# Kernel optimization log

Measured on AMD Instinct MI355X. Metric: run time of the kernel, lower is better.

Reference implementation:

```python
import jax, jax.numpy as jnp
import numpy as np

N_EMBD = 1024
NUM_EXPERTS = 8
TOP_K = 2
HIDDEN = 2048  # n_embd * hidden_mult(2)
AUX_COEF = 0.01
B, S = 4, 2048


def setup_inputs() -> dict:
    key = jax.random.key(0)
    k_x, k_g, k_w1, k_w2 = jax.random.split(key, 4)
    x = jax.random.normal(k_x, (B, S, N_EMBD), dtype=jnp.float32)
    # router gate: Linear(n_embd, num_experts, bias=False) -> weight (E, D), applied as x @ W^T
    gate_w = jax.random.uniform(k_g, (NUM_EXPERTS, N_EMBD), dtype=jnp.float32,
                                minval=-1.0 / np.sqrt(N_EMBD), maxval=1.0 / np.sqrt(N_EMBD))
    w1 = jax.random.uniform(k_w1, (NUM_EXPERTS, N_EMBD, HIDDEN), dtype=jnp.float32,
                            minval=-1.0 / np.sqrt(N_EMBD), maxval=1.0 / np.sqrt(N_EMBD))
    w2 = jax.random.uniform(k_w2, (NUM_EXPERTS, HIDDEN, N_EMBD), dtype=jnp.float32,
                            minval=-1.0 / np.sqrt(HIDDEN), maxval=1.0 / np.sqrt(HIDDEN))
    return {"x": x, "gate_w": gate_w, "w1": w1, "w2": w2}


def reference(x, gate_w, w1, w2):
    batch, seq, d = x.shape
    # router (token-level, no noise / eval path)
    router_logits = jnp.einsum('bsd,ed->bse', x, gate_w)          # (B,S,E)
    router_probs = jax.nn.softmax(router_logits, axis=-1)
    top_k_probs, top_k_indices = jax.lax.top_k(router_probs, TOP_K)  # (B,S,K)
    top_k_probs = top_k_probs / jnp.sum(top_k_probs, axis=-1, keepdims=True)

    # dense all-expert FFN (matches torch einsum pattern)
    x_flat = x.reshape(-1, d)                                      # (N,D), N=B*S
    hidden = jnp.einsum('nd,edh->neh', x_flat, w1)                 # (N,E,H)
    hidden = jax.nn.relu(hidden)
    expert_out = jnp.einsum('neh,ehd->ned', hidden, w2)            # (N,E,D)
    expert_out = expert_out.reshape(batch, seq, NUM_EXPERTS, d)    # (B,S,E,D)

    # gather selected experts and combine
    idx = top_k_indices[..., None]                                 # (B,S,K,1)
    selected = jnp.take_along_axis(expert_out, idx, axis=2)        # (B,S,K,D)
    output = jnp.sum(selected * top_k_probs[..., None], axis=2)    # (B,S,D)

    # load-balancing aux loss (Switch style)
    probs_flat = router_probs.reshape(-1, NUM_EXPERTS)             # (N,E)
    top_expert = jnp.argmax(probs_flat, axis=-1)                   # (N,)
    f = jnp.mean(jax.nn.one_hot(top_expert, NUM_EXPERTS, dtype=probs_flat.dtype), axis=0)
    P = jnp.mean(probs_flat, axis=0)
    aux_loss = AUX_COEF * NUM_EXPERTS * jnp.sum(f * P)
    return output, aux_loss
```

## Files before the change

kernel.cpp:

```cpp
#include <hip/hip_runtime.h>
#include <hip/hip_bf16.h>
#include <stdint.h>

#define N_TOK 8192
#define DIM   1024
#define HID   2048
#define NEXP  8
#define RB    256

typedef __bf16 bf16x8 __attribute__((ext_vector_type(8)));
typedef float  f32x4  __attribute__((ext_vector_type(4)));
typedef unsigned short u16x8 __attribute__((ext_vector_type(8)));
typedef unsigned short u16x4 __attribute__((ext_vector_type(4)));

__device__ __forceinline__ float bits2f(unsigned short u) {
    union { unsigned int i; float f; } c; c.i = ((unsigned int)u) << 16; return c.f;
}
__device__ __forceinline__ unsigned short f2bfbits(float f) {
    __hip_bfloat16 h = __float2bfloat16(f);
    return *(unsigned short*)&h;
}

__device__ __forceinline__ void load_lds16(const void* g, void* l) {
    __builtin_amdgcn_global_load_lds(
        (const __attribute__((address_space(1))) void*)g,
        (__attribute__((address_space(3))) void*)l,
        16, 0, 0);
}

__global__ __launch_bounds__(512) void route_k(
    const float* __restrict__ x,
    const float* __restrict__ gate,
    int* __restrict__ epack, float* __restrict__ pw,
    unsigned short* __restrict__ xb,
    int* __restrict__ H0, int* __restrict__ H1, float* __restrict__ Pblk)
{
    __shared__ float gwS[NEXP][16][64];
    __shared__ int h0S[NEXP], h1S[NEXP];
    __shared__ float pS[NEXP];
    int tid = threadIdx.x;
    if (tid < NEXP) { h0S[tid] = 0; h1S[tid] = 0; pS[tid] = 0.f; }
    for (int idx = tid; idx < NEXP * DIM; idx += 512) {
        int e = idx >> 10, rem = idx & 1023, i = rem >> 6, l = rem & 63;
        gwS[e][i][l] = gate[e * DIM + l * 16 + i];
    }
    __syncthreads();
    int w = tid >> 6, lane = tid & 63;
    float prAcc[NEXP];
    #pragma unroll
    for (int e = 0; e < NEXP; ++e) prAcc[e] = 0.f;
    for (int it = 0; it < 4; ++it) {
        int token = blockIdx.x * 32 + w * 4 + it;
        const float* xr = x + (size_t)token * DIM + lane * 16;
        float xv[16];
        #pragma unroll
        for (int q = 0; q < 4; ++q) {
            float4 v = *(const float4*)(xr + q * 4);
            xv[q * 4 + 0] = v.x; xv[q * 4 + 1] = v.y; xv[q * 4 + 2] = v.z; xv[q * 4 + 3] = v.w;
        }
        {
            u16x8 o0, o1;
            #pragma unroll
            for (int i = 0; i < 8; ++i) { o0[i] = f2bfbits(xv[i]); o1[i] = f2bfbits(xv[8 + i]); }
            unsigned short* dst = xb + (size_t)token * DIM + lane * 16;
            *(u16x8*)dst = o0;
            *(u16x8*)(dst + 8) = o1;
        }
        float lg[NEXP];
        #pragma unroll
        for (int e = 0; e < NEXP; ++e) {
            float s = 0.f;
            #pragma unroll
            for (int i = 0; i < 16; ++i) s += xv[i] * gwS[e][i][lane];
            lg[e] = s;
        }
        #pragma unroll
        for (int off = 32; off > 0; off >>= 1)
            #pragma unroll
            for (int e = 0; e < NEXP; ++e) lg[e] += __shfl_xor(lg[e], off);
        float mx = lg[0]; int am = 0;
        #pragma unroll
        for (int e = 1; e < NEXP; ++e) if (lg[e] > mx) { mx = lg[e]; am = e; }
        float pr[NEXP], se = 0.f;
        #pragma unroll
        for (int e = 0; e < NEXP; ++e) { pr[e] = __expf(lg[e] - mx); se += pr[e]; }
        float inv = 1.f / se;
        #pragma unroll
        for (int e = 0; e < NEXP; ++e) pr[e] *= inv;
        float m2 = -1.f; int a2 = 0;
        #pragma unroll
        for (int e = 0; e < NEXP; ++e) if (e != am && pr[e] > m2) { m2 = pr[e]; a2 = e; }
        float psum = pr[am] + m2;
        if (lane == 0) {
            epack[token] = am | (a2 << 4);
            pw[token * 2] = pr[am] / psum;
            pw[token * 2 + 1] = m2 / psum;
            atomicAdd(&h0S[am], 1);
            atomicAdd(&h1S[a2], 1);
            #pragma unroll
            for (int e = 0; e < NEXP; ++e) prAcc[e] += pr[e];
        }
    }
    if (lane == 0) {
        #pragma unroll
        for (int e = 0; e < NEXP; ++e) atomicAdd(&pS[e], prAcc[e]);
    }
    __syncthreads();
    if (tid < NEXP) {
        H0[blockIdx.x * NEXP + tid] = h0S[tid];
        H1[blockIdx.x * NEXP + tid] = h1S[tid];
        Pblk[blockIdx.x * NEXP + tid] = pS[tid];
    }
}

__global__ __launch_bounds__(256) void scan_k(
    const int* __restrict__ H0, const int* __restrict__ H1,
    const float* __restrict__ Pblk,
    int* __restrict__ bbL, int* __restrict__ counts, int* __restrict__ basep,
    float* __restrict__ aux)
{
    __shared__ int h0S[RB * NEXP], h1S[RB * NEXP], bbS[RB * NEXP];
    __shared__ float pSh[RB * NEXP];
    __shared__ int cS[NEXP], fS[NEXP];
    __shared__ float psS[NEXP];
    int tid = threadIdx.x;
    for (int i = tid; i < RB * NEXP; i += 256) { h0S[i] = H0[i]; h1S[i] = H1[i]; pSh[i] = Pblk[i]; }
    __syncthreads();
    if (tid < NEXP) {
        int run = 0, f = 0; float p = 0.f;
        for (int b = 0; b < RB; ++b) {
            int i = b * NEXP + tid;
            bbS[i] = run;
            run += h0S[i] + h1S[i];
            f += h0S[i];
            p += pSh[i];
        }
        cS[tid] = run; fS[tid] = f; psS[tid] = p;
        counts[tid] = run;
    }
    __syncthreads();
    if (tid == 0) {
        int b = 0; float s = 0.f;
        for (int e = 0; e < NEXP; ++e) {
            basep[e] = b; b += cS[e];
            s += (fS[e] * (1.f / 8192.f)) * (psS[e] * (1.f / 8192.f));
        }
        aux[0] = 0.01f * 8.f * s;
    }
    __syncthreads();
    for (int i = tid; i < RB * NEXP; i += 256) bbL[i] = bbS[i];
}

__global__ __launch_bounds__(256) void scatter_k(
    const int* __restrict__ epack, const int* __restrict__ bbL,
    int* __restrict__ tok_list, int* __restrict__ code)
{
    int tid = threadIdx.x;
    int w = tid >> 6, lane = tid & 63;
    int g = blockIdx.x * 4 + w;
    int token = g * 32 + (lane >> 1);
    int ep = epack[token];
    int e = (lane & 1) ? ((ep >> 4) & 0xF) : (ep & 0xF);
    unsigned long long lower = (lane == 0) ? 0ull : ((~0ull) >> (64 - lane));
    unsigned long long mymask = 0;
    #pragma unroll
    for (int ee = 0; ee < NEXP; ++ee) {
        unsigned long long m = __ballot(e == ee);
        if (ee == e) mymask = m;
    }
    int rank = __popcll(mymask & lower);
    int slot = bbL[g * NEXP + e] + rank;
    tok_list[e * N_TOK + slot] = token;
    code[token * 2 + (lane & 1)] = (e << 13) | slot;
}

__global__ __launch_bounds__(256) void transpose_cvt_k(const float* __restrict__ in,
                                                       unsigned short* __restrict__ out,
                                                       int R, int C)
{
    __shared__ unsigned short tile[64][72];
    int e = blockIdx.z;
    const float* inp = in + (size_t)e * R * C;
    unsigned short* outp = out + (size_t)e * R * C;
    int r0 = blockIdx.y * 64, c0 = blockIdx.x * 64;
    int tid = threadIdx.x;
    {
        int r = tid >> 2;
        int cseg = (tid & 3) * 16;
        const float* src = inp + (size_t)(r0 + r) * C + c0 + cseg;
        #pragma unroll
        for (int q = 0; q < 4; ++q) {
            float4 v = *(const float4*)(src + q * 4);
            tile[r][cseg + q * 4 + 0] = f2bfbits(v.x);
            tile[r][cseg + q * 4 + 1] = f2bfbits(v.y);
            tile[r][cseg + q * 4 + 2] = f2bfbits(v.z);
            tile[r][cseg + q * 4 + 3] = f2bfbits(v.w);
        }
    }
    __syncthreads();
    {
        int c = tid >> 2;
        int rseg = (tid & 3) * 16;
        unsigned short* dst = outp + (size_t)(c0 + c) * R + r0 + rseg;
        #pragma unroll
        for (int h = 0; h < 2; ++h) {
            u16x8 o;
            #pragma unroll
            for (int i = 0; i < 8; ++i) o[i] = tile[rseg + h * 8 + i][c];
            *(u16x8*)(dst + h * 8) = o;
        }
    }
}

template<bool GATHER, bool RELU, bool SPLITK>
__global__ __launch_bounds__(256) void moe_gemm(
    const unsigned short* __restrict__ A,
    const unsigned short* __restrict__ B,
    unsigned short* __restrict__ O0,
    unsigned short* __restrict__ O1,
    const int* __restrict__ counts,
    const int* __restrict__ basep,
    const int* __restrict__ tok_list,
    const int K, const int N)
{
    int e, koff, steps;
    unsigned short* O;
    if (SPLITK) {
        e = blockIdx.z >> 1;
        int kp = blockIdx.z & 1;
        koff = kp * (K >> 1);
        steps = K >> 6;
        O = kp ? O1 : O0;
    } else {
        e = blockIdx.z; koff = 0; steps = K >> 5; O = O0;
    }
    const int cnt = counts[e];
    const int m0 = blockIdx.y * 128;
    if (m0 >= cnt) return;
    const int n0 = blockIdx.x * 128;
    const int bas = basep[e];

    const int tid = threadIdx.x;
    const int w = tid >> 6, lane = tid & 63;
    const int wr = w >> 1, wc = w & 1;

    __shared__ __align__(16) unsigned short lds[8192];

    const int kc = ((tid & 3) ^ ((tid >> 3) & 3)) * 8;
    const int r0i = tid >> 2, r1i = 64 + (tid >> 2);
    const unsigned short *aRow0, *aRow1;
    if (GATHER) {
        int s0 = m0 + r0i, s1 = m0 + r1i;
        int t0 = (s0 < cnt) ? tok_list[e * N_TOK + s0] : 0;
        int t1 = (s1 < cnt) ? tok_list[e * N_TOK + s1] : 0;
        aRow0 = A + (size_t)t0 * K + koff + kc;
        aRow1 = A + (size_t)t1 * K + koff + kc;
    } else {
        int s0 = m0 + r0i; if (s0 > cnt - 1) s0 = cnt - 1;
        int s1 = m0 + r1i; if (s1 > cnt - 1) s1 = cnt - 1;
        aRow0 = A + (size_t)(bas + s0) * K + koff + kc;
        aRow1 = A + (size_t)(bas + s1) * K + koff + kc;
    }
    const unsigned short* Be = B + (size_t)e * N * K;
    const unsigned short* bRow0 = Be + (size_t)(n0 + r0i) * K + koff + kc;
    const unsigned short* bRow1 = Be + (size_t)(n0 + r1i) * K + koff + kc;

    f32x4 acc[4][4];
    #pragma unroll
    for (int i = 0; i < 4; ++i)
        #pragma unroll
        for (int j = 0; j < 4; ++j) acc[i][j] = f32x4{0.f, 0.f, 0.f, 0.f};

    const int quad = lane >> 4, ml = lane & 15;
    unsigned short* ldsA0 = &lds[tid * 8];
    unsigned short* ldsA1 = &lds[2048 + tid * 8];
    unsigned short* ldsB0 = &lds[4096 + tid * 8];
    unsigned short* ldsB1 = &lds[6144 + tid * 8];

    int offA[4], offB[4];
    #pragma unroll
    for (int i = 0; i < 4; ++i) {
        int Ra = wr * 64 + i * 16 + ml;
        offA[i] = Ra * 32 + ((quad ^ ((Ra >> 1) & 3)) * 8);
        int Rb = wc * 64 + i * 16 + ml;
        offB[i] = 4096 + Rb * 32 + ((quad ^ ((Rb >> 1) & 3)) * 8);
    }

    for (int kt = 0; kt < steps; ++kt) {
        const int ko = kt * 32;
        load_lds16(aRow0 + ko, ldsA0);
        load_lds16(aRow1 + ko, ldsA1);
        load_lds16(bRow0 + ko, ldsB0);
        load_lds16(bRow1 + ko, ldsB1);
        __syncthreads();
        bf16x8 af[4], bfr[4];
        #pragma unroll
        for (int i = 0; i < 4; ++i) af[i] = *(const bf16x8*)&lds[offA[i]];
        #pragma unroll
        for (int j = 0; j < 4; ++j) bfr[j] = *(const bf16x8*)&lds[offB[j]];
        #pragma unroll
        for (int i = 0; i < 4; ++i)
            #pragma unroll
            for (int j = 0; j < 4; ++j)
                acc[i][j] = __builtin_amdgcn_mfma_f32_16x16x32_bf16(af[i], bfr[j], acc[i][j], 0, 0, 0);
        __syncthreads();
    }

    #pragma unroll
    for (int i = 0; i < 4; ++i) {
        int rbase = wr * 64 + i * 16 + quad * 4;
        #pragma unroll
        for (int r = 0; r < 4; ++r) {
            int slot = m0 + rbase + r;
            if (slot < cnt) {
                unsigned short* orow = O + (size_t)(bas + slot) * N + n0 + wc * 64 + ml;
                #pragma unroll
                for (int j = 0; j < 4; ++j) {
                    float v = acc[i][j][r];
                    if (RELU) v = v > 0.f ? v : 0.f;
                    orow[j * 16] = f2bfbits(v);
                }
            }
        }
    }
}

__global__ __launch_bounds__(256) void combine_k(
    const unsigned short* __restrict__ Y0,
    const unsigned short* __restrict__ Y1,
    const int* __restrict__ code, const float* __restrict__ pw,
    const int* __restrict__ basep,
    float* __restrict__ out)
{
    int t = blockIdx.x;
    int c0 = code[t * 2], c1 = code[t * 2 + 1];
    float p0 = pw[t * 2], p1 = pw[t * 2 + 1];
    size_t r0 = (size_t)(basep[c0 >> 13] + (c0 & 0x1FFF)) * DIM;
    size_t r1 = (size_t)(basep[c1 >> 13] + (c1 & 0x1FFF)) * DIM;
    int d = threadIdx.x * 4;
    u16x4 a0 = *(const u16x4*)(Y0 + r0 + d);
    u16x4 a1 = *(const u16x4*)(Y1 + r0 + d);
    u16x4 b0 = *(const u16x4*)(Y0 + r1 + d);
    u16x4 b1 = *(const u16x4*)(Y1 + r1 + d);
    float4 o;
    o.x = p0 * (bits2f(a0[0]) + bits2f(a1[0])) + p1 * (bits2f(b0[0]) + bits2f(b1[0]));
    o.y = p0 * (bits2f(a0[1]) + bits2f(a1[1])) + p1 * (bits2f(b0[1]) + bits2f(b1[1]));
    o.z = p0 * (bits2f(a0[2]) + bits2f(a1[2])) + p1 * (bits2f(b0[2]) + bits2f(b1[2]));
    o.w = p0 * (bits2f(a0[3]) + bits2f(a1[3])) + p1 * (bits2f(b0[3]) + bits2f(b1[3]));
    *(float4*)(out + (size_t)t * DIM + d) = o;
}

extern "C" void kernel_launch(void* const* d_in, const int* in_sizes, int n_in,
                              void* d_out, int out_size, void* d_ws, size_t ws_size,
                              hipStream_t stream)
{
    const float* x    = (const float*)d_in[0];
    const float* gate = (const float*)d_in[1];
    const float* w1   = (const float*)d_in[2];
    const float* w2   = (const float*)d_in[3];
    float* out = (float*)d_out;

    char* ws = (char*)d_ws;
    int*   counts   = (int*)(ws + 0);
    int*   basep    = (int*)(ws + 256);
    int*   epack    = (int*)(ws + 1024);
    int*   H0       = (int*)(ws + 1024 + 32768);
    int*   H1       = (int*)(ws + 1024 + 40960);
    float* Pblk     = (float*)(ws + 1024 + 49152);
    int*   bbL      = (int*)(ws + 1024 + 57344);
    int*   tok_list = (int*)(ws + 131072);
    int*   code     = (int*)(ws + 131072 + 262144);
    float* pw       = (float*)(ws + 131072 + 262144 + 65536);
    unsigned short* w1t    = (unsigned short*)(ws + (1 << 20));
    unsigned short* w2t    = (unsigned short*)(ws + (1 << 20) + 33554432);
    unsigned short* hidden = (unsigned short*)(ws + (1 << 20) + 67108864);
    unsigned short* xb     = (unsigned short*)(ws + (1 << 20) + 134217728);
    unsigned short* Yp0    = xb;
    unsigned short* Yp1    = w1t;

    route_k<<<RB, 512, 0, stream>>>(x, gate, epack, pw, xb, H0, H1, Pblk);
    scan_k<<<1, 256, 0, stream>>>(H0, H1, Pblk, bbL, counts, basep, out + (size_t)N_TOK * DIM);
    scatter_k<<<64, 256, 0, stream>>>(epack, bbL, tok_list, code);
    transpose_cvt_k<<<dim3(HID / 64, DIM / 64, NEXP), 256, 0, stream>>>(w1, w1t, DIM, HID);
    transpose_cvt_k<<<dim3(DIM / 64, HID / 64, NEXP), 256, 0, stream>>>(w2, w2t, HID, DIM);
    moe_gemm<true, true, false><<<dim3(HID / 128, 64, NEXP), 256, 0, stream>>>(
        xb, w1t, hidden, nullptr, counts, basep, tok_list, DIM, HID);
    moe_gemm<false, false, true><<<dim3(DIM / 128, 64, NEXP * 2), 256, 0, stream>>>(
        hidden, w2t, Yp0, Yp1, counts, basep, tok_list, HID, DIM);
    combine_k<<<N_TOK, 256, 0, stream>>>(Yp0, Yp1, code, pw, basep, out);
}
```

Baseline: 428.8 us.

## Fuse routing with weight transposes and pipeline GEMM loads with double-buffered LDS

Routing and both weight transpose/bf16 conversions are merged into one kernel launch so they share a grid and drop two launches. The MoE GEMM gets a double-buffered 64-wide K pipeline using async global-to-LDS loads with explicit vmcnt waits, raw barriers and MFMA priority boosting. Split-K on the second GEMM is removed, so combine reads one partial instead of two. The larger LDS (64KB) limits occupancy, and dropping split-K halves the grid for the down projection.

Result: faster. 399.0 us (-7.0%).

```diff
diff --git a/kernel.cpp b/kernel.cpp
--- a/kernel.cpp
+++ b/kernel.cpp
@@ -28,88 +28,137 @@
         16, 0, 0);
 }
 
-__global__ __launch_bounds__(512) void route_k(
+__global__ __launch_bounds__(256) void fused_pre_k(
     const float* __restrict__ x,
     const float* __restrict__ gate,
+    const float* __restrict__ w1,
+    const float* __restrict__ w2,
     int* __restrict__ epack, float* __restrict__ pw,
     unsigned short* __restrict__ xb,
-    int* __restrict__ H0, int* __restrict__ H1, float* __restrict__ Pblk)
-{
-    __shared__ float gwS[NEXP][16][64];
-    __shared__ int h0S[NEXP], h1S[NEXP];
-    __shared__ float pS[NEXP];
-    int tid = threadIdx.x;
-    if (tid < NEXP) { h0S[tid] = 0; h1S[tid] = 0; pS[tid] = 0.f; }
-    for (int idx = tid; idx < NEXP * DIM; idx += 512) {
-        int e = idx >> 10, rem = idx & 1023, i = rem >> 6, l = rem & 63;
-        gwS[e][i][l] = gate[e * DIM + l * 16 + i];
+    int* __restrict__ H0, int* __restrict__ H1, float* __restrict__ Pblk,
+    unsigned short* __restrict__ w1t, unsigned short* __restrict__ w2t)
+{
+    __shared__ __align__(16) union {
+        struct { float gw[NEXP][16][64]; int h0[NEXP]; int h1[NEXP]; float p[NEXP]; } r;
+        unsigned short tile[64][72];
+    } S;
+    const int tid = threadIdx.x;
+    const int bx  = blockIdx.x;
+
+    if (bx < RB) {
+        if (tid < NEXP) { S.r.h0[tid] = 0; S.r.h1[tid] = 0; S.r.p[tid] = 0.f; }
+        for (int idx = tid; idx < NEXP * DIM; idx += 256) {
+            int e = idx >> 10, rem = idx & 1023, i = rem >> 6, l = rem & 63;
+            S.r.gw[e][i][l] = gate[e * DIM + l * 16 + i];
+        }
+        __syncthreads();
+        int w = tid >> 6, lane = tid & 63;
+        float prAcc[NEXP];
+        #pragma unroll
+        for (int e = 0; e < NEXP; ++e) prAcc[e] = 0.f;
+        for (int it = 0; it < 8; ++it) {
+            int token = bx * 32 + w * 8 + it;
+            const float* xr = x + (size_t)token * DIM + lane * 16;
+            float xv[16];
+            #pragma unroll
+            for (int q = 0; q < 4; ++q) {
+                float4 v = *(const float4*)(xr + q * 4);
+                xv[q * 4 + 0] = v.x; xv[q * 4 + 1] = v.y; xv[q * 4 + 2] = v.z; xv[q * 4 + 3] = v.w;
+            }
+            {
+                u16x8 o0, o1;
+                #pragma unroll
+                for (int i = 0; i < 8; ++i) { o0[i] = f2bfbits(xv[i]); o1[i] = f2bfbits(xv[8 + i]); }
+                unsigned short* dst = xb + (size_t)token * DIM + lane * 16;
+                *(u16x8*)dst = o0;
+                *(u16x8*)(dst + 8) = o1;
+            }
+            float lg[NEXP];
+            #pragma unroll
+            for (int e = 0; e < NEXP; ++e) {
+                float s = 0.f;
+                #pragma unroll
+                for (int i = 0; i < 16; ++i) s += xv[i] * S.r.gw[e][i][lane];
+                lg[e] = s;
+            }
+            #pragma unroll
+            for (int off = 32; off > 0; off >>= 1)
+                #pragma unroll
+                for (int e = 0; e < NEXP; ++e) lg[e] += __shfl_xor(lg[e], off);
+            float mx = lg[0]; int am = 0;
+            #pragma unroll
+            for (int e = 1; e < NEXP; ++e) if (lg[e] > mx) { mx = lg[e]; am = e; }
+            float pr[NEXP], se = 0.f;
+            #pragma unroll
+            for (int e = 0; e < NEXP; ++e) { pr[e] = __expf(lg[e] - mx); se += pr[e]; }
+            float inv = 1.f / se;
+            #pragma unroll
+            for (int e = 0; e < NEXP; ++e) pr[e] *= inv;
+            float m2 = -1.f; int a2 = 0;
+            #pragma unroll
+            for (int e = 0; e < NEXP; ++e) if (e != am && pr[e] > m2) { m2 = pr[e]; a2 = e; }
+            float psum = pr[am] + m2;
+            if (lane == 0) {
+                epack[token] = am | (a2 << 4);
+                pw[token * 2] = pr[am] / psum;
+                pw[token * 2 + 1] = m2 / psum;
+                atomicAdd(&S.r.h0[am], 1);
+                atomicAdd(&S.r.h1[a2], 1);
+                #pragma unroll
+                for (int e = 0; e < NEXP; ++e) prAcc[e] += pr[e];
+            }
+        }
+        if (lane == 0) {
+            #pragma unroll
+            for (int e = 0; e < NEXP; ++e) atomicAdd(&S.r.p[e], prAcc[e]);
+        }
+        __syncthreads();
+        if (tid < NEXP) {
+            H0[bx * NEXP + tid] = S.r.h0[tid];
+            H1[bx * NEXP + tid] = S.r.h1[tid];
+            Pblk[bx * NEXP + tid] = S.r.p[tid];
+        }
+        return;
+    }
+
+    int bT = bx - RB;
+    const float* inp; unsigned short* outp;
+    int R, C, r0, c0;
+    if (bT < 4096) {
+        int e = bT >> 9, rem = bT & 511;
+        R = DIM; C = HID;
+        inp = w1 + (size_t)e * R * C; outp = w1t + (size_t)e * R * C;
+        r0 = (rem >> 5) << 6; c0 = (rem & 31) << 6;
+    } else {
+        int b2 = bT - 4096;
+        int e = b2 >> 9, rem = b2 & 511;
+        R = HID; C = DIM;
+        inp = w2 + (size_t)e * R * C; outp = w2t + (size_t)e * R * C;
+        r0 = (rem >> 4) << 6; c0 = (rem & 15) << 6;
+    }
+    {
+        int r = tid >> 2, cseg = (tid & 3) * 16;
+        const float* src = inp + (size_t)(r0 + r) * C + c0 + cseg;
+        #pragma unroll
+        for (int q = 0; q < 4; ++q) {
+            float4 v = *(const float4*)(src + q * 4);
+            S.tile[r][cseg + q * 4 + 0] = f2bfbits(v.x);
+            S.tile[r][cseg + q * 4 + 1] = f2bfbits(v.y);
+            S.tile[r][cseg + q * 4 + 2] = f2bfbits(v.z);
+            S.tile[r][cseg + q * 4 + 3] = f2bfbits(v.w);
+        }
     }
     __syncthreads();
-    int w = tid >> 6, lane = tid & 63;
-    float prAcc[NEXP];
-    #pragma unroll
-    for (int e = 0; e < NEXP; ++e) prAcc[e] = 0.f;
-    for (int it = 0; it < 4; ++it) {
-        int token = blockIdx.x * 32 + w * 4 + it;
-        const float* xr = x + (size_t)token * DIM + lane * 16;
-        float xv[16];
-        #pragma unroll
-        for (int q = 0; q < 4; ++q) {
-            float4 v = *(const float4*)(xr + q * 4);
-            xv[q * 4 + 0] = v.x; xv[q * 4 + 1] = v.y; xv[q * 4 + 2] = v.z; xv[q * 4 + 3] = v.w;
-        }
-        {
-            u16x8 o0, o1;
-            #pragma unroll
-            for (int i = 0; i < 8; ++i) { o0[i] = f2bfbits(xv[i]); o1[i] = f2bfbits(xv[8 + i]); }
-            unsigned short* dst = xb + (size_t)token * DIM + lane * 16;
-            *(u16x8*)dst = o0;
-            *(u16x8*)(dst + 8) = o1;
-        }
-        float lg[NEXP];
-        #pragma unroll
-        for (int e = 0; e < NEXP; ++e) {
-            float s = 0.f;
-            #pragma unroll
-            for (int i = 0; i < 16; ++i) s += xv[i] * gwS[e][i][lane];
-            lg[e] = s;
-        }
-        #pragma unroll
-        for (int off = 32; off > 0; off >>= 1)
-            #pragma unroll
-            for (int e = 0; e < NEXP; ++e) lg[e] += __shfl_xor(lg[e], off);
-        float mx = lg[0]; int am = 0;
-        #pragma unroll
-        for (int e = 1; e < NEXP; ++e) if (lg[e] > mx) { mx = lg[e]; am = e; }
-        float pr[NEXP], se = 0.f;
-        #pragma unroll
-        for (int e = 0; e < NEXP; ++e) { pr[e] = __expf(lg[e] - mx); se += pr[e]; }
-        float inv = 1.f / se;
-        #pragma unroll
-        for (int e = 0; e < NEXP; ++e) pr[e] *= inv;
-        float m2 = -1.f; int a2 = 0;
-        #pragma unroll
-        for (int e = 0; e < NEXP; ++e) if (e != am && pr[e] > m2) { m2 = pr[e]; a2 = e; }
-        float psum = pr[am] + m2;
-        if (lane == 0) {
-            epack[token] = am | (a2 << 4);
-            pw[token * 2] = pr[am] / psum;
-            pw[token * 2 + 1] = m2 / psum;
-            atomicAdd(&h0S[am], 1);
-            atomicAdd(&h1S[a2], 1);
-            #pragma unroll
-            for (int e = 0; e < NEXP; ++e) prAcc[e] += pr[e];
-        }
-    }
-    if (lane == 0) {
-        #pragma unroll
-        for (int e = 0; e < NEXP; ++e) atomicAdd(&pS[e], prAcc[e]);
-    }
-    __syncthreads();
-    if (tid < NEXP) {
-        H0[blockIdx.x * NEXP + tid] = h0S[tid];
-        H1[blockIdx.x * NEXP + tid] = h1S[tid];
-        Pblk[blockIdx.x * NEXP + tid] = pS[tid];
+    {
+        int c = tid >> 2, rseg = (tid & 3) * 16;
+        unsigned short* dst = outp + (size_t)(c0 + c) * R + r0 + rseg;
+        #pragma unroll
+        for (int h = 0; h < 2; ++h) {
+            u16x8 o;
+            #pragma unroll
+            for (int i = 0; i < 8; ++i) o[i] = S.tile[rseg + h * 8 + i][c];
+            *(u16x8*)(dst + h * 8) = o;
+        }
     }
 }
 
@@ -174,66 +223,21 @@
     code[token * 2 + (lane & 1)] = (e << 13) | slot;
 }
 
-__global__ __launch_bounds__(256) void transpose_cvt_k(const float* __restrict__ in,
-                                                       unsigned short* __restrict__ out,
-                                                       int R, int C)
-{
-    __shared__ unsigned short tile[64][72];
-    int e = blockIdx.z;
-    const float* inp = in + (size_t)e * R * C;
-    unsigned short* outp = out + (size_t)e * R * C;
-    int r0 = blockIdx.y * 64, c0 = blockIdx.x * 64;
-    int tid = threadIdx.x;
-    {
-        int r = tid >> 2;
-        int cseg = (tid & 3) * 16;
-        const float* src = inp + (size_t)(r0 + r) * C + c0 + cseg;
-        #pragma unroll
-        for (int q = 0; q < 4; ++q) {
-            float4 v = *(const float4*)(src + q * 4);
-            tile[r][cseg + q * 4 + 0] = f2bfbits(v.x);
-            tile[r][cseg + q * 4 + 1] = f2bfbits(v.y);
-            tile[r][cseg + q * 4 + 2] = f2bfbits(v.z);
-            tile[r][cseg + q * 4 + 3] = f2bfbits(v.w);
-        }
-    }
-    __syncthreads();
-    {
-        int c = tid >> 2;
-        int rseg = (tid & 3) * 16;
-        unsigned short* dst = outp + (size_t)(c0 + c) * R + r0 + rseg;
-        #pragma unroll
-        for (int h = 0; h < 2; ++h) {
-            u16x8 o;
-            #pragma unroll
-            for (int i = 0; i < 8; ++i) o[i] = tile[rseg + h * 8 + i][c];
-            *(u16x8*)(dst + h * 8) = o;
-        }
-    }
-}
-
-template<bool GATHER, bool RELU, bool SPLITK>
-__global__ __launch_bounds__(256) void moe_gemm(
+#define VMW(Nv) asm volatile("s_waitcnt vmcnt(" #Nv ")" ::: "memory")
+#define BARv()  asm volatile("s_barrier" ::: "memory")
+
+template<bool GATHER, bool RELU, int KT>
+__global__ __launch_bounds__(256, 2) void moe_gemm(
     const unsigned short* __restrict__ A,
     const unsigned short* __restrict__ B,
-    unsigned short* __restrict__ O0,
-    unsigned short* __restrict__ O1,
+    unsigned short* __restrict__ O,
     const int* __restrict__ counts,
     const int* __restrict__ basep,
     const int* __restrict__ tok_list,
-    const int K, const int N)
-{
-    int e, koff, steps;
-    unsigned short* O;
-    if (SPLITK) {
-        e = blockIdx.z >> 1;
-        int kp = blockIdx.z & 1;
-        koff = kp * (K >> 1);
-        steps = K >> 6;
-        O = kp ? O1 : O0;
-    } else {
-        e = blockIdx.z; koff = 0; steps = K >> 5; O = O0;
-    }
+    const int N)
+{
+    constexpr int K = KT * 64;
+    const int e = blockIdx.z;
     const int cnt = counts[e];
     const int m0 = blockIdx.y * 128;
     if (m0 >= cnt) return;
@@ -244,7 +248,7 @@
     const int w = tid >> 6, lane = tid & 63;
     const int wr = w >> 1, wc = w & 1;
 
-    __shared__ __align__(16) unsigned short lds[8192];
+    __shared__ __align__(16) unsigned short lds[32768];
 
     const int kc = ((tid & 3) ^ ((tid >> 3) & 3)) * 8;
     const int r0i = tid >> 2, r1i = 64 + (tid >> 2);
@@ -253,17 +257,17 @@
         int s0 = m0 + r0i, s1 = m0 + r1i;
         int t0 = (s0 < cnt) ? tok_list[e * N_TOK + s0] : 0;
         int t1 = (s1 < cnt) ? tok_list[e * N_TOK + s1] : 0;
-        aRow0 = A + (size_t)t0 * K + koff + kc;
-        aRow1 = A + (size_t)t1 * K + koff + kc;
+        aRow0 = A + (size_t)t0 * K + kc;
+        aRow1 = A + (size_t)t1 * K + kc;
     } else {
         int s0 = m0 + r0i; if (s0 > cnt - 1) s0 = cnt - 1;
         int s1 = m0 + r1i; if (s1 > cnt - 1) s1 = cnt - 1;
-        aRow0 = A + (size_t)(bas + s0) * K + koff + kc;
-        aRow1 = A + (size_t)(bas + s1) * K + koff + kc;
+        aRow0 = A + (size_t)(bas + s0) * K + kc;
+        aRow1 = A + (size_t)(bas + s1) * K + kc;
     }
     const unsigned short* Be = B + (size_t)e * N * K;
-    const unsigned short* bRow0 = Be + (size_t)(n0 + r0i) * K + koff + kc;
-    const unsigned short* bRow1 = Be + (size_t)(n0 + r1i) * K + koff + kc;
+    const unsigned short* bRow0 = Be + (size_t)(n0 + r0i) * K + kc;
+    const unsigned short* bRow1 = Be + (size_t)(n0 + r1i) * K + kc;
 
     f32x4 acc[4][4];
     #pragma unroll
@@ -272,38 +276,56 @@
         for (int j = 0; j < 4; ++j) acc[i][j] = f32x4{0.f, 0.f, 0.f, 0.f};
 
     const int quad = lane >> 4, ml = lane & 15;
-    unsigned short* ldsA0 = &lds[tid * 8];
-    unsigned short* ldsA1 = &lds[2048 + tid * 8];
-    unsigned short* ldsB0 = &lds[4096 + tid * 8];
-    unsigned short* ldsB1 = &lds[6144 + tid * 8];
-
     int offA[4], offB[4];
     #pragma unroll
     for (int i = 0; i < 4; ++i) {
         int Ra = wr * 64 + i * 16 + ml;
         offA[i] = Ra * 32 + ((quad ^ ((Ra >> 1) & 3)) * 8);
         int Rb = wc * 64 + i * 16 + ml;
-        offB[i] = 4096 + Rb * 32 + ((quad ^ ((Rb >> 1) & 3)) * 8);
-    }
-
-    for (int kt = 0; kt < steps; ++kt) {
-        const int ko = kt * 32;
-        load_lds16(aRow0 + ko, ldsA0);
-        load_lds16(aRow1 + ko, ldsA1);
-        load_lds16(bRow0 + ko, ldsB0);
-        load_lds16(bRow1 + ko, ldsB1);
-        __syncthreads();
+        offB[i] = Rb * 32 + ((quad ^ ((Rb >> 1) & 3)) * 8);
+    }
+
+    auto stageG = [&](int tt, int h) {
+        const int db = ((tt & 1) << 14) + (h << 12) + (tid << 3);
+        const int toff = tt * 64 + h * 32;
+        load_lds16(aRow0 + toff, &lds[db]);
+        load_lds16(aRow1 + toff, &lds[db + 2048]);
+        load_lds16(bRow0 + toff, &lds[db + 8192]);
+        load_lds16(bRow1 + toff, &lds[db + 8192 + 2048]);
+    };
+
+    auto compute = [&](int bb, int ks) {
+        const unsigned short* Lb = &lds[(bb << 14) + (ks << 12)];
         bf16x8 af[4], bfr[4];
         #pragma unroll
-        for (int i = 0; i < 4; ++i) af[i] = *(const bf16x8*)&lds[offA[i]];
-        #pragma unroll
-        for (int j = 0; j < 4; ++j) bfr[j] = *(const bf16x8*)&lds[offB[j]];
+        for (int i = 0; i < 4; ++i) af[i] = *(const bf16x8*)&Lb[offA[i]];
+        #pragma unroll
+        for (int j = 0; j < 4; ++j) bfr[j] = *(const bf16x8*)&Lb[8192 + offB[j]];
+        __builtin_amdgcn_s_setprio(1);
         #pragma unroll
         for (int i = 0; i < 4; ++i)
             #pragma unroll
             for (int j = 0; j < 4; ++j)
                 acc[i][j] = __builtin_amdgcn_mfma_f32_16x16x32_bf16(af[i], bfr[j], acc[i][j], 0, 0, 0);
-        __syncthreads();
+        __builtin_amdgcn_s_setprio(0);
+        BARv();
+    };
+
+    stageG(0, 0); stageG(0, 1); stageG(1, 0);
+
+    #pragma unroll 2
+    for (int t = 0; t < KT - 2; ++t) {
+        const int b = t & 1;
+        stageG(t + 1, 1); VMW(12); BARv(); compute(b, 0);
+        stageG(t + 2, 0); VMW(12); BARv(); compute(b, 1);
+    }
+    {
+        const int bA = (KT - 2) & 1;
+        stageG(KT - 1, 1); VMW(12); BARv(); compute(bA, 0);
+        VMW(8);  BARv(); compute(bA, 1);
+        const int bB = (KT - 1) & 1;
+        VMW(4);  BARv(); compute(bB, 0);
+        VMW(0);  BARv(); compute(bB, 1);
     }
 
     #pragma unroll
@@ -326,8 +348,7 @@
 }
 
 __global__ __launch_bounds__(256) void combine_k(
-    const unsigned short* __restrict__ Y0,
-    const unsigned short* __restrict__ Y1,
+    const unsigned short* __restrict__ Y,
     const int* __restrict__ code, const float* __restrict__ pw,
     const int* __restrict__ basep,
     float* __restrict__ out)
@@ -338,15 +359,13 @@
     size_t r0 = (size_t)(basep[c0 >> 13] + (c0 & 0x1FFF)) * DIM;
     size_t r1 = (size_t)(basep[c1 >> 13] + (c1 & 0x1FFF)) * DIM;
     int d = threadIdx.x * 4;
-    u16x4 a0 = *(const u16x4*)(Y0 + r0 + d);
-    u16x4 a1 = *(const u16x4*)(Y1 + r0 + d);
-    u16x4 b0 = *(const u16x4*)(Y0 + r1 + d);
-    u16x4 b1 = *(const u16x4*)(Y1 + r1 + d);
+    u16x4 a = *(const u16x4*)(Y + r0 + d);
+    u16x4 b = *(const u16x4*)(Y + r1 + d);
     float4 o;
-    o.x = p0 * (bits2f(a0[0]) + bits2f(a1[0])) + p1 * (bits2f(b0[0]) + bits2f(b1[0]));
-    o.y = p0 * (bits2f(a0[1]) + bits2f(a1[1])) + p1 * (bits2f(b0[1]) + bits2f(b1[1]));
-    o.z = p0 * (bits2f(a0[2]) + bits2f(a1[2])) + p1 * (bits2f(b0[2]) + bits2f(b1[2]));
-    o.w = p0 * (bits2f(a0[3]) + bits2f(a1[3])) + p1 * (bits2f(b0[3]) + bits2f(b1[3]));
+    o.x = p0 * bits2f(a[0]) + p1 * bits2f(b[0]);
+    o.y = p0 * bits2f(a[1]) + p1 * bits2f(b[1]);
+    o.z = p0 * bits2f(a[2]) + p1 * bits2f(b[2]);
+    o.w = p0 * bits2f(a[3]) + p1 * bits2f(b[3]);
     *(float4*)(out + (size_t)t * DIM + d) = o;
 }
 
@@ -375,17 +394,15 @@
     unsigned short* w2t    = (unsigned short*)(ws + (1 << 20) + 33554432);
     unsigned short* hidden = (unsigned short*)(ws + (1 << 20) + 67108864);
     unsigned short* xb     = (unsigned short*)(ws + (1 << 20) + 134217728);
-    unsigned short* Yp0    = xb;
-    unsigned short* Yp1    = w1t;
-
-    route_k<<<RB, 512, 0, stream>>>(x, gate, epack, pw, xb, H0, H1, Pblk);
+    unsigned short* Y      = xb;
+
+    fused_pre_k<<<RB + 8192, 256, 0, stream>>>(x, gate, w1, w2, epack, pw, xb,
+                                               H0, H1, Pblk, w1t, w2t);
     scan_k<<<1, 256, 0, stream>>>(H0, H1, Pblk, bbL, counts, basep, out + (size_t)N_TOK * DIM);
     scatter_k<<<64, 256, 0, stream>>>(epack, bbL, tok_list, code);
-    transpose_cvt_k<<<dim3(HID / 64, DIM / 64, NEXP), 256, 0, stream>>>(w1, w1t, DIM, HID);
-    transpose_cvt_k<<<dim3(DIM / 64, HID / 64, NEXP), 256, 0, stream>>>(w2, w2t, HID, DIM);
-    moe_gemm<true, true, false><<<dim3(HID / 128, 64, NEXP), 256, 0, stream>>>(
-        xb, w1t, hidden, nullptr, counts, basep, tok_list, DIM, HID);
-    moe_gemm<false, false, true><<<dim3(DIM / 128, 64, NEXP * 2), 256, 0, stream>>>(
-        hidden, w2t, Yp0, Yp1, counts, basep, tok_list, HID, DIM);
-    combine_k<<<N_TOK, 256, 0, stream>>>(Yp0, Yp1, code, pw, basep, out);
-}
+    moe_gemm<true, true, DIM / 64><<<dim3(HID / 128, 64, NEXP), 256, 0, stream>>>(
+        xb, w1t, hidden, counts, basep, tok_list, HID);
+    moe_gemm<false, false, HID / 64><<<dim3(DIM / 128, 64, NEXP), 256, 0, stream>>>(
+        hidden, w2t, Y, counts, basep, tok_list, DIM);
+    combine_k<<<N_TOK, 256, 0, stream>>>(Y, code, pw, basep, out);
+}
```
